# Kernel tuning notes

Measured on AMD Instinct MI355X. Metric: run time of the kernel, lower is better.

The kernel has to match this reference:

```python
import jax, jax.numpy as jnp
import numpy as np

BATCH = 4096
IN_CAPS = 64
OUT_CAPS = 16
IN_DIM = 64
OUT_DIM = 64
NUM_ITER = 3
LN_EPS = 1e-5


def setup_inputs() -> dict:
    key = jax.random.key(0)
    ks = jax.random.split(key, 13)
    n = lambda k, s: jax.random.normal(k, s, dtype=jnp.float32)
    return {
        "x_inp": n(ks[0], (BATCH, IN_CAPS, IN_DIM)),
        "W_A": n(ks[1], (IN_CAPS, IN_DIM)),
        "B_A": n(ks[2], (IN_CAPS,)),
        "W_F1": n(ks[3], (IN_CAPS, IN_DIM, IN_DIM)),
        "W_F2": n(ks[4], (OUT_CAPS, IN_DIM, OUT_DIM)),
        "B_F2": n(ks[5], (OUT_CAPS, OUT_DIM)),
        "W_G1": n(ks[6], (OUT_DIM, OUT_DIM)),
        "W_G2": n(ks[7], (OUT_CAPS, OUT_DIM, IN_DIM)),
        "B_G2": n(ks[8], (OUT_CAPS, IN_DIM)),
        "ln_gamma": jnp.ones((OUT_DIM,), jnp.float32),
        "ln_beta": jnp.zeros((OUT_DIM,), jnp.float32),
        "W_S": n(ks[9], (IN_CAPS, OUT_CAPS, IN_DIM)),
        "B_S": n(ks[10], (IN_CAPS, OUT_CAPS)),
        "beta_use": n(ks[11], (IN_CAPS, OUT_CAPS)),
        "beta_ign": n(ks[12], (IN_CAPS, OUT_CAPS)),
    }


def _layer_norm(x, gamma, beta):
    mu = jnp.mean(x, axis=-1, keepdims=True)
    var = jnp.var(x, axis=-1, keepdims=True)  # biased, matches torch LayerNorm
    return (x - mu) * jax.lax.rsqrt(var + LN_EPS) * gamma + beta


def reference(x_inp, W_A, B_A, W_F1, W_F2, B_F2, W_G1, W_G2, B_G2,
              ln_gamma, ln_beta, W_S, B_S, beta_use, beta_ign):
    B = x_inp.shape[0]
    inv_sqrt = np.float32(1.0 / np.sqrt(IN_DIM))
    # activation logits per input capsule: [B, in_caps]
    a_e = jnp.einsum('bif,if->bi', x_inp, W_A) * inv_sqrt + B_A
    f_a_e = jax.nn.sigmoid(a_e)  # loop-invariant
    # temp_F is loop-invariant: [B, in_caps, in_dim]
    temp_F = jnp.einsum('bif,ifh->bih', x_inp, W_F1) * inv_sqrt
    R_em = jnp.full((B, IN_CAPS, OUT_CAPS), 1.0 / OUT_CAPS, dtype=x_inp.dtype)
    x_out = None
    for _ in range(NUM_ITER):
        D_use = f_a_e[:, :, None] * R_em                      # [B,i,m]
        D_ign = f_a_e[:, :, None] - D_use                     # [B,i,m]
        phi_em = beta_use * D_use - beta_ign * D_ign          # [B,i,m]
        temp_F_routed = phi_em.sum(axis=-1)[:, :, None] * temp_F  # [B,i,h]
        x_out = jnp.einsum('bih,mhd->bmd', temp_F_routed, W_F2) + B_F2  # [B,m,d]
        x_out_norm = _layer_norm(x_out, ln_gamma, ln_beta)
        temp_G = jnp.einsum('bmd,dh->bmh', x_out_norm, W_G1)  # [B,m,d]
        x_inp_hat = jnp.einsum('bmh,mhi->bmi', temp_G, W_G2) + B_G2  # [B,m,f]
        consistency = jnp.einsum('bif,bmf,imf->bim', x_inp, x_inp_hat, W_S) + B_S
        R_em = jax.nn.softmax(consistency, axis=-1)  # exp(log_softmax)
    return x_out
```

## Files before the change

kernel.cpp:

```cpp
#include <hip/hip_runtime.h>
#include <math.h>

#define IC 64
#define OC 16
#define DIM 64

typedef __attribute__((ext_vector_type(8))) short bf16x8;
typedef __attribute__((ext_vector_type(4))) float f32x4;

__device__ __forceinline__ unsigned short f2bf(float f) {
    unsigned int b = __float_as_uint(f);
    b += 0x7fffu + ((b >> 16) & 1u);
    return (unsigned short)(b >> 16);
}
__device__ __forceinline__ float bf2f(unsigned short h) {
    return __uint_as_float(((unsigned int)h) << 16);
}

__global__ void kSetup(const float* __restrict__ W_F2, const float* __restrict__ W_S,
                       const float* __restrict__ B_S, const float* __restrict__ bu,
                       const float* __restrict__ bi_, const float* __restrict__ W_G1,
                       const float* __restrict__ W_G2,
                       float* __restrict__ WF2t, float* __restrict__ WSt2,
                       float* __restrict__ WG12,
                       float* __restrict__ BSt, float* __restrict__ cb,
                       float* __restrict__ db, float* __restrict__ eb)
{
    int e = blockIdx.x * 256 + threadIdx.x;
    {
        int h = e >> 10, m = (e >> 6) & 15, d = e & 63;
        WF2t[e] = W_F2[((size_t)m * 64 + h) * 64 + d];
    }
    {
        int m = e >> 12, fo = (e >> 8) & 15, i = (e >> 2) & 63, fi = e & 3;
        WSt2[e] = W_S[((size_t)i * 16 + m) * 64 + fo * 4 + fi];
    }
    {
        int m = e >> 12, d = (e >> 6) & 63, f = e & 63;
        const float* g1 = W_G1 + d * 64;
        const float* g2 = W_G2 + (size_t)m * 4096 + f;
        float a = 0.f;
#pragma unroll 8
        for (int h = 0; h < 64; h++) a += g1[h] * g2[h * 64];
        WG12[e] = a;
    }
    if (e < 1024) {
        int m = e >> 6, i = e & 63;
        BSt[e] = B_S[i * 16 + m];
        cb[e] = bu[e] + bi_[e];
    }
    if (e < 64) {
        float sc = 0.f, sd = 0.f;
        for (int m = 0; m < 16; m++) {
            sc += bu[e * 16 + m] + bi_[e * 16 + m];
            sd += bi_[e * 16 + m];
        }
        db[e] = sd;
        eb[e] = sc * (1.0f / 16.0f) - sd;
    }
}

__global__ __launch_bounds__(256, 4)
void kT(const float* __restrict__ x, const float* __restrict__ W_A,
        const float* __restrict__ B_A, const float* __restrict__ eb,
        float* __restrict__ xq, float* __restrict__ fa, float* __restrict__ phi)
{
    __shared__ float Xs[2 * 64 * 65];
    const int t = threadIdx.x;
    const int blk = blockIdx.x;

    const float4* x4 = (const float4*)x;
#pragma unroll
    for (int s = 0; s < 8; s++) {
        int p = s * 256 + t;
        float4 v = x4[(size_t)blk * 2048 + p];
        int b = p >> 10, i = (p >> 4) & 63, fo = p & 15;
        float* row = &Xs[(b * 64 + i) * 65 + fo * 4];
        row[0] = v.x; row[1] = v.y; row[2] = v.z; row[3] = v.w;
    }
    __syncthreads();

    const int lane = t & 63, w = t >> 6;
#pragma unroll
    for (int s = 0; s < 8; s++) {
        int idx = s * 4 + w;
        int b = idx >> 4, fo = idx & 15;
        const float* row = &Xs[(b * 64 + lane) * 65 + fo * 4];
        ((float4*)xq)[((size_t)(blk * 2 + b) * 16 + fo) * 64 + lane] =
            make_float4(row[0], row[1], row[2], row[3]);
    }

    {
        int p = t >> 1, h = t & 1;
        int b = p >> 6, i = p & 63;
        const float* row = &Xs[(b * 64 + i) * 65 + h * 32];
        const float* wa = W_A + i * 64 + h * 32;
        float v = 0.f;
#pragma unroll
        for (int j = 0; j < 32; j++) v += row[j] * wa[j];
        v += __shfl_xor(v, 1);
        if (h == 0) {
            float ae = v * 0.125f + B_A[i];
            float fv = 1.0f / (1.0f + expf(-ae));
            size_t o = (size_t)(blk * 2 + b) * 64 + i;
            fa[o] = fv;
            phi[o] = fv * eb[i];
        }
    }
}

__global__ __launch_bounds__(256, 4)
void kA(const float* __restrict__ x, const float* __restrict__ W_F1,
        float* __restrict__ tF)
{
    __shared__ unsigned short Ah[64][72], Al[64][72];
    __shared__ unsigned short Bh[64][72], Bl[64][72];
    const int i = blockIdx.y;
    const int b0 = blockIdx.x * 64;
    const int t = threadIdx.x;
    const int bl = t >> 2, q = t & 3;

    {
        const float* src = x + ((size_t)(b0 + bl) * IC + i) * DIM + q * 4;
#pragma unroll
        for (int j4 = 0; j4 < 4; j4++) {
            float4 v = *(const float4*)(src + j4 * 16);
            int f = q * 4 + j4 * 16;
            float vv[4] = {v.x, v.y, v.z, v.w};
            ushort4 h4, l4;
            unsigned short hh;
            hh = f2bf(vv[0]); h4.x = hh; l4.x = f2bf(vv[0] - bf2f(hh));
            hh = f2bf(vv[1]); h4.y = hh; l4.y = f2bf(vv[1] - bf2f(hh));
            hh = f2bf(vv[2]); h4.z = hh; l4.z = f2bf(vv[2] - bf2f(hh));
            hh = f2bf(vv[3]); h4.w = hh; l4.w = f2bf(vv[3] - bf2f(hh));
            *(ushort4*)&Ah[bl][f] = h4;
            *(ushort4*)&Al[bl][f] = l4;
        }
        const float* wsrc = W_F1 + ((size_t)i * DIM + bl) * DIM + q * 4;
#pragma unroll
        for (int j4 = 0; j4 < 4; j4++) {
            float4 v = *(const float4*)(wsrc + j4 * 16);
            int h0 = q * 4 + j4 * 16;
            float vv[4] = {v.x, v.y, v.z, v.w};
#pragma unroll
            for (int c = 0; c < 4; c++) {
                unsigned short hh = f2bf(vv[c]);
                Bh[h0 + c][bl] = hh;
                Bl[h0 + c][bl] = f2bf(vv[c] - bf2f(hh));
            }
        }
    }
    __syncthreads();

    const int w = t >> 6, lane = t & 63;
    const int fm = lane & 15, fq = lane >> 4;
    const int r0 = w * 16;
    f32x4 acc[4];
#pragma unroll
    for (int nt = 0; nt < 4; nt++) {
        acc[nt][0] = 0.f; acc[nt][1] = 0.f; acc[nt][2] = 0.f; acc[nt][3] = 0.f;
    }

#pragma unroll
    for (int ks = 0; ks < 2; ks++) {
        const int kk = ks * 32 + fq * 8;
        bf16x8 ah = *(const bf16x8*)&Ah[r0 + fm][kk];
        bf16x8 al = *(const bf16x8*)&Al[r0 + fm][kk];
#pragma unroll
        for (int nt = 0; nt < 4; nt++) {
            bf16x8 bh = *(const bf16x8*)&Bh[nt * 16 + fm][kk];
            bf16x8 bl2 = *(const bf16x8*)&Bl[nt * 16 + fm][kk];
            acc[nt] = __builtin_amdgcn_mfma_f32_16x16x32_bf16(ah, bh, acc[nt], 0, 0, 0);
            acc[nt] = __builtin_amdgcn_mfma_f32_16x16x32_bf16(ah, bl2, acc[nt], 0, 0, 0);
            acc[nt] = __builtin_amdgcn_mfma_f32_16x16x32_bf16(al, bh, acc[nt], 0, 0, 0);
        }
    }

#pragma unroll
    for (int nt = 0; nt < 4; nt++)
#pragma unroll
        for (int j = 0; j < 4; j++) {
            int row = r0 + fq * 4 + j;
            int col = nt * 16 + fm;
            tF[((size_t)(b0 + row) * IC + i) * DIM + col] = acc[nt][j] * 0.125f;
        }
}

__global__ __launch_bounds__(256, 4)
void kS(const float* __restrict__ phi, const float* __restrict__ tF,
        float* __restrict__ s)
{
    __shared__ float ph[4 * 64];
    const int t = threadIdx.x;
    const int b0 = blockIdx.x * 4;
    ph[t] = phi[(size_t)b0 * 64 + t];
    __syncthreads();

    const int w = t >> 6, lane = t & 63;
    const int ig = lane >> 4, hq = lane & 15;
    const int b = b0 + w;
    const float4* tf4 = (const float4*)(tF + ((size_t)b * 64 + ig * 16) * 64) + hq;
    float4 a = make_float4(0.f, 0.f, 0.f, 0.f);
#pragma unroll
    for (int k = 0; k < 16; k++) {
        float p = ph[w * 64 + ig * 16 + k];
        float4 v = tf4[k * 16];
        a.x += p * v.x; a.y += p * v.y; a.z += p * v.z; a.w += p * v.w;
    }
#pragma unroll
    for (int k = 16; k <= 32; k <<= 1) {
        a.x += __shfl_xor(a.x, k); a.y += __shfl_xor(a.y, k);
        a.z += __shfl_xor(a.z, k); a.w += __shfl_xor(a.w, k);
    }
    if (ig == 0)
        ((float4*)(s + (size_t)b * 64))[hq] = a;
}

__global__ __launch_bounds__(256, 4)
void kXG(const float* __restrict__ s, const float* __restrict__ WF2t,
         const float* __restrict__ B_F2, const float* __restrict__ WG12,
         const float* __restrict__ B_G2,
         const float* __restrict__ gam, const float* __restrict__ bet,
         float* __restrict__ xhat, float* __restrict__ out, const int last)
{
    __shared__ float A[64][68];
    __shared__ float Wb[64][68];
    const int b0 = blockIdx.x * 64;
    const int m = blockIdx.y;
    const int t = threadIdx.x;
    const int bl = t >> 2, q = t & 3;
    const int tr = t >> 4, tc = t & 15;

    {
        const float* src = s + (size_t)(b0 + bl) * DIM + q * 4;
#pragma unroll
        for (int j4 = 0; j4 < 4; j4++) {
            float4 v = *(const float4*)(src + j4 * 16);
            int f = q * 4 + j4 * 16;
            A[f + 0][bl] = v.x; A[f + 1][bl] = v.y;
            A[f + 2][bl] = v.z; A[f + 3][bl] = v.w;
        }
        const float* wsrc = WF2t + ((size_t)bl * OC + m) * DIM + q * 4;
#pragma unroll
        for (int j4 = 0; j4 < 4; j4++)
            *(float4*)&Wb[bl][q * 4 + j4 * 16] = *(const float4*)(wsrc + j4 * 16);
    }
    __syncthreads();

    float acc[4][4];
#pragma unroll
    for (int r = 0; r < 4; r++)
#pragma unroll
        for (int c = 0; c < 4; c++) acc[r][c] = 0.f;
#pragma unroll 8
    for (int k = 0; k < 64; k++) {
        float4 a = *(const float4*)&A[k][tr * 4];
        float4 w = *(const float4*)&Wb[k][tc * 4];
        float ar[4] = {a.x, a.y, a.z, a.w};
#pragma unroll
        for (int r = 0; r < 4; r++) {
            acc[r][0] += ar[r] * w.x; acc[r][1] += ar[r] * w.y;
            acc[r][2] += ar[r] * w.z; acc[r][3] += ar[r] * w.w;
        }
    }
    {
        float4 bf = *(const float4*)&B_F2[m * DIM + tc * 4];
#pragma unroll
        for (int r = 0; r < 4; r++) {
            acc[r][0] += bf.x; acc[r][1] += bf.y;
            acc[r][2] += bf.z; acc[r][3] += bf.w;
        }
    }
    if (last) {
#pragma unroll
        for (int r = 0; r < 4; r++)
            *(float4*)&out[((size_t)(b0 + tr * 4 + r) * OC + m) * DIM + tc * 4] =
                make_float4(acc[r][0], acc[r][1], acc[r][2], acc[r][3]);
        return;
    }
    {
        float4 gv = *(const float4*)&gam[tc * 4];
        float4 bv = *(const float4*)&bet[tc * 4];
#pragma unroll
        for (int r = 0; r < 4; r++) {
            float sum = acc[r][0] + acc[r][1] + acc[r][2] + acc[r][3];
            float sq = acc[r][0] * acc[r][0] + acc[r][1] * acc[r][1] +
                       acc[r][2] * acc[r][2] + acc[r][3] * acc[r][3];
#pragma unroll
            for (int k = 1; k <= 8; k <<= 1) {
                sum += __shfl_xor(sum, k);
                sq  += __shfl_xor(sq, k);
            }
            float mu = sum * (1.0f / 64.0f);
            float var = sq * (1.0f / 64.0f) - mu * mu;
            float rs = 1.0f / sqrtf(var + 1e-5f);
            acc[r][0] = (acc[r][0] - mu) * rs * gv.x + bv.x;
            acc[r][1] = (acc[r][1] - mu) * rs * gv.y + bv.y;
            acc[r][2] = (acc[r][2] - mu) * rs * gv.z + bv.z;
            acc[r][3] = (acc[r][3] - mu) * rs * gv.w + bv.w;
        }
    }
    __syncthreads();
    {
#pragma unroll
        for (int r = 0; r < 4; r++)
#pragma unroll
            for (int c = 0; c < 4; c++)
                A[tc * 4 + c][tr * 4 + r] = acc[r][c];
        const float* wsrc = WG12 + ((size_t)m * DIM + bl) * DIM + q * 4;
#pragma unroll
        for (int j4 = 0; j4 < 4; j4++)
            *(float4*)&Wb[bl][q * 4 + j4 * 16] = *(const float4*)(wsrc + j4 * 16);
    }
    __syncthreads();

    float xh[4][4];
    {
        float4 bg = *(const float4*)&B_G2[m * DIM + tc * 4];
#pragma unroll
        for (int r = 0; r < 4; r++) {
            xh[r][0] = bg.x; xh[r][1] = bg.y; xh[r][2] = bg.z; xh[r][3] = bg.w;
        }
    }
#pragma unroll 8
    for (int k = 0; k < 64; k++) {
        float4 a = *(const float4*)&A[k][tr * 4];
        float4 w = *(const float4*)&Wb[k][tc * 4];
        float ar[4] = {a.x, a.y, a.z, a.w};
#pragma unroll
        for (int r = 0; r < 4; r++) {
            xh[r][0] += ar[r] * w.x; xh[r][1] += ar[r] * w.y;
            xh[r][2] += ar[r] * w.z; xh[r][3] += ar[r] * w.w;
        }
    }
#pragma unroll
    for (int r = 0; r < 4; r++)
        *(float4*)&xhat[((size_t)(b0 + tr * 4 + r) * OC + m) * DIM + tc * 4] =
            make_float4(xh[r][0], xh[r][1], xh[r][2], xh[r][3]);
}

__global__ __launch_bounds__(256, 4)
void kC(const float* __restrict__ xq, const float* __restrict__ xhat,
        const float* __restrict__ WSt2, const float* __restrict__ BSt,
        const float* __restrict__ cb, const float* __restrict__ db,
        const float* __restrict__ fa, const float* __restrict__ tF,
        float* __restrict__ s)
{
    __shared__ float buf[4 * 64 * 17];
    __shared__ float phs[4][64];
    const int b0 = blockIdx.x * 4;
    const int t = threadIdx.x;
    const int w = t >> 6, lane = t & 63;

    {
        const float4* src = (const float4*)(xhat + (size_t)b0 * OC * DIM);
        float4* dst = (float4*)buf;
#pragma unroll
        for (int j = 0; j < 4; j++) dst[t + j * 256] = src[t + j * 256];
    }
    __syncthreads();

    float acc[4][4];
#pragma unroll
    for (int k = 0; k < 4; k++) {
        float bs = BSt[(w * 4 + k) * IC + lane];
#pragma unroll
        for (int g = 0; g < 4; g++) acc[g][k] = bs;
    }

    const float4* xq4 = (const float4*)xq;
    for (int fc = 0; fc < 64; fc += 8) {
        const int fo = fc >> 2;
        float wreg[4][8];
#pragma unroll
        for (int k = 0; k < 4; k++) {
            int m = w * 4 + k;
#pragma unroll
            for (int q2 = 0; q2 < 2; q2++) {
                float4 v = *(const float4*)&WSt2[(((size_t)m * 16 + fo + q2) * IC + lane) * 4];
                wreg[k][q2 * 4 + 0] = v.x; wreg[k][q2 * 4 + 1] = v.y;
                wreg[k][q2 * 4 + 2] = v.z; wreg[k][q2 * 4 + 3] = v.w;
            }
        }
#pragma unroll
        for (int g = 0; g < 4; g++) {
            float xr[8];
#pragma unroll
            for (int q2 = 0; q2 < 2; q2++) {
                float4 v = xq4[((size_t)(b0 + g) * 16 + fo + q2) * 64 + lane];
                xr[q2 * 4 + 0] = v.x; xr[q2 * 4 + 1] = v.y;
                xr[q2 * 4 + 2] = v.z; xr[q2 * 4 + 3] = v.w;
            }
#pragma unroll
            for (int k = 0; k < 4; k++) {
                int m = w * 4 + k;
                const float* hp = &buf[(g * OC + m) * DIM + fc];
                float hr[8];
#pragma unroll
                for (int q2 = 0; q2 < 2; q2++) {
                    float4 v = *(const float4*)(hp + q2 * 4);
                    hr[q2 * 4 + 0] = v.x; hr[q2 * 4 + 1] = v.y;
                    hr[q2 * 4 + 2] = v.z; hr[q2 * 4 + 3] = v.w;
                }
#pragma unroll
                for (int ff = 0; ff < 8; ff++)
                    acc[g][k] += xr[ff] * hr[ff] * wreg[k][ff];
            }
        }
    }
    __syncthreads();
#pragma unroll
    for (int g = 0; g < 4; g++)
#pragma unroll
        for (int k = 0; k < 4; k++)
            buf[(g * IC + lane) * 17 + w * 4 + k] = acc[g][k];
    __syncthreads();

    {
        int g = t >> 6, i = t & 63;
        const float* row = &buf[(g * IC + i) * 17];
        float v[16], mx = -1e30f;
#pragma unroll
        for (int m = 0; m < OC; m++) { v[m] = row[m]; mx = fmaxf(mx, v[m]); }
        float sum = 0.f;
#pragma unroll
        for (int m = 0; m < OC; m++) { v[m] = expf(v[m] - mx); sum += v[m]; }
        float inv = 1.0f / sum;
        float a2 = 0.f;
#pragma unroll
        for (int m = 0; m < OC; m++) a2 += v[m] * inv * cb[i * OC + m];
        phs[g][i] = fa[(size_t)(b0 + g) * IC + i] * (a2 - db[i]);
    }
    __syncthreads();

    {
        const int ig = lane >> 4, hq = lane & 15;
        const int b = b0 + w;
        const float4* tf4 = (const float4*)(tF + ((size_t)b * 64 + ig * 16) * 64) + hq;
        float4 a = make_float4(0.f, 0.f, 0.f, 0.f);
#pragma unroll
        for (int k = 0; k < 16; k++) {
            float p = phs[w][ig * 16 + k];
            float4 v = tf4[k * 16];
            a.x += p * v.x; a.y += p * v.y; a.z += p * v.z; a.w += p * v.w;
        }
#pragma unroll
        for (int k = 16; k <= 32; k <<= 1) {
            a.x += __shfl_xor(a.x, k); a.y += __shfl_xor(a.y, k);
            a.z += __shfl_xor(a.z, k); a.w += __shfl_xor(a.w, k);
        }
        if (ig == 0)
            ((float4*)(s + (size_t)b * 64))[hq] = a;
    }
}

extern "C" void kernel_launch(void* const* d_in, const int* in_sizes, int n_in,
                              void* d_out, int out_size, void* d_ws, size_t ws_size,
                              hipStream_t stream)
{
    const float* x    = (const float*)d_in[0];
    const float* W_A  = (const float*)d_in[1];
    const float* B_A  = (const float*)d_in[2];
    const float* W_F1 = (const float*)d_in[3];
    const float* W_F2 = (const float*)d_in[4];
    const float* B_F2 = (const float*)d_in[5];
    const float* W_G1 = (const float*)d_in[6];
    const float* W_G2 = (const float*)d_in[7];
    const float* B_G2 = (const float*)d_in[8];
    const float* gam  = (const float*)d_in[9];
    const float* bet  = (const float*)d_in[10];
    const float* W_S  = (const float*)d_in[11];
    const float* B_S  = (const float*)d_in[12];
    const float* bu   = (const float*)d_in[13];
    const float* bi_  = (const float*)d_in[14];

    float* ws   = (float*)d_ws;
    float* tF   = ws;
    float* xq   = tF + 16777216;
    float* fa   = xq + 16777216;
    float* phi  = fa + 262144;
    float* s    = phi + 262144;
    float* xhat = s + 262144;
    float* WF2t = xhat + 4194304;
    float* WSt2 = WF2t + 65536;
    float* WG12 = WSt2 + 65536;
    float* BSt  = WG12 + 65536;
    float* cb   = BSt + 1024;
    float* db   = cb + 1024;
    float* eb   = db + 64;
    float* out  = (float*)d_out;

    kSetup<<<256, 256, 0, stream>>>(W_F2, W_S, B_S, bu, bi_, W_G1, W_G2,
                                    WF2t, WSt2, WG12, BSt, cb, db, eb);
    kT<<<2048, 256, 0, stream>>>(x, W_A, B_A, eb, xq, fa, phi);
    kA<<<dim3(64, 64), 256, 0, stream>>>(x, W_F1, tF);
    kS<<<1024, 256, 0, stream>>>(phi, tF, s);
    for (int it = 0; it < 3; ++it) {
        kXG<<<dim3(64, 16), 256, 0, stream>>>(s, WF2t, B_F2, WG12, B_G2,
                                              gam, bet, xhat, out, it == 2 ? 1 : 0);
        if (it < 2)
            kC<<<1024, 256, 0, stream>>>(xq, xhat, WSt2, BSt, cb, db, fa, tF, s);
    }
}
```

Before: 307.7 us.

## Run kXG GEMMs on MFMA using split-bf16 (hi/lo) three-term emulation

Replaces the FP32 scalar FMA loops in kXG with bf16 MFMA 16x16x32 instructions. Each fp32 operand is split into high and low bf16 halves, and three products (hh, hl, lh) recover near-fp32 accuracy. The setup kernel now pre-splits and transposes W_F2 and the fused W_G1·W_G2 weights into bf16 hi/lo buffers. The aim is to cut ALU time in the per-iteration GEMMs, at the cost of extra conversion work and some loss of precision in the dropped lo·lo term.

```diff
diff --git a/kernel.cpp b/kernel.cpp
--- a/kernel.cpp
+++ b/kernel.cpp
@@ -21,15 +21,19 @@
                        const float* __restrict__ B_S, const float* __restrict__ bu,
                        const float* __restrict__ bi_, const float* __restrict__ W_G1,
                        const float* __restrict__ W_G2,
-                       float* __restrict__ WF2t, float* __restrict__ WSt2,
-                       float* __restrict__ WG12,
+                       float* __restrict__ WSt2,
+                       unsigned short* __restrict__ W1h, unsigned short* __restrict__ W1l,
+                       unsigned short* __restrict__ W2h, unsigned short* __restrict__ W2l,
                        float* __restrict__ BSt, float* __restrict__ cb,
                        float* __restrict__ db, float* __restrict__ eb)
 {
     int e = blockIdx.x * 256 + threadIdx.x;
     {
         int h = e >> 10, m = (e >> 6) & 15, d = e & 63;
-        WF2t[e] = W_F2[((size_t)m * 64 + h) * 64 + d];
+        float v = W_F2[((size_t)m * 64 + h) * 64 + d];
+        unsigned short hh = f2bf(v);
+        size_t o = ((size_t)m * 64 + d) * 64 + h;
+        W1h[o] = hh; W1l[o] = f2bf(v - bf2f(hh));
     }
     {
         int m = e >> 12, fo = (e >> 8) & 15, i = (e >> 2) & 63, fi = e & 3;
@@ -42,7 +46,9 @@
         float a = 0.f;
 #pragma unroll 8
         for (int h = 0; h < 64; h++) a += g1[h] * g2[h * 64];
-        WG12[e] = a;
+        unsigned short hh = f2bf(a);
+        size_t o = ((size_t)m * 64 + f) * 64 + d;
+        W2h[o] = hh; W2l[o] = f2bf(a - bf2f(hh));
     }
     if (e < 1024) {
         int m = e >> 6, i = e & 63;
@@ -217,75 +223,98 @@
 }
 
 __global__ __launch_bounds__(256, 4)
-void kXG(const float* __restrict__ s, const float* __restrict__ WF2t,
-         const float* __restrict__ B_F2, const float* __restrict__ WG12,
+void kXG(const float* __restrict__ s,
+         const unsigned short* __restrict__ W1h, const unsigned short* __restrict__ W1l,
+         const float* __restrict__ B_F2,
+         const unsigned short* __restrict__ W2h, const unsigned short* __restrict__ W2l,
          const float* __restrict__ B_G2,
          const float* __restrict__ gam, const float* __restrict__ bet,
          float* __restrict__ xhat, float* __restrict__ out, const int last)
 {
-    __shared__ float A[64][68];
-    __shared__ float Wb[64][68];
+    __shared__ unsigned short Ah[64][72], Al[64][72];
+    __shared__ unsigned short Bh[64][72], Bl[64][72];
     const int b0 = blockIdx.x * 64;
     const int m = blockIdx.y;
     const int t = threadIdx.x;
     const int bl = t >> 2, q = t & 3;
-    const int tr = t >> 4, tc = t & 15;
-
-    {
-        const float* src = s + (size_t)(b0 + bl) * DIM + q * 4;
+
+    {
+        const float* src = s + (size_t)(b0 + bl) * DIM + q * 16;
 #pragma unroll
         for (int j4 = 0; j4 < 4; j4++) {
-            float4 v = *(const float4*)(src + j4 * 16);
-            int f = q * 4 + j4 * 16;
-            A[f + 0][bl] = v.x; A[f + 1][bl] = v.y;
-            A[f + 2][bl] = v.z; A[f + 3][bl] = v.w;
-        }
-        const float* wsrc = WF2t + ((size_t)bl * OC + m) * DIM + q * 4;
-#pragma unroll
-        for (int j4 = 0; j4 < 4; j4++)
-            *(float4*)&Wb[bl][q * 4 + j4 * 16] = *(const float4*)(wsrc + j4 * 16);
-    }
-    __syncthreads();
-
-    float acc[4][4];
-#pragma unroll
-    for (int r = 0; r < 4; r++)
-#pragma unroll
-        for (int c = 0; c < 4; c++) acc[r][c] = 0.f;
-#pragma unroll 8
-    for (int k = 0; k < 64; k++) {
-        float4 a = *(const float4*)&A[k][tr * 4];
-        float4 w = *(const float4*)&Wb[k][tc * 4];
-        float ar[4] = {a.x, a.y, a.z, a.w};
-#pragma unroll
-        for (int r = 0; r < 4; r++) {
-            acc[r][0] += ar[r] * w.x; acc[r][1] += ar[r] * w.y;
-            acc[r][2] += ar[r] * w.z; acc[r][3] += ar[r] * w.w;
-        }
-    }
-    {
-        float4 bf = *(const float4*)&B_F2[m * DIM + tc * 4];
-#pragma unroll
-        for (int r = 0; r < 4; r++) {
-            acc[r][0] += bf.x; acc[r][1] += bf.y;
-            acc[r][2] += bf.z; acc[r][3] += bf.w;
-        }
-    }
+            float4 v = ((const float4*)src)[j4];
+            int f = q * 16 + j4 * 4;
+            float vv[4] = {v.x, v.y, v.z, v.w};
+            ushort4 h4, l4;
+            unsigned short hh;
+            hh = f2bf(vv[0]); h4.x = hh; l4.x = f2bf(vv[0] - bf2f(hh));
+            hh = f2bf(vv[1]); h4.y = hh; l4.y = f2bf(vv[1] - bf2f(hh));
+            hh = f2bf(vv[2]); h4.z = hh; l4.z = f2bf(vv[2] - bf2f(hh));
+            hh = f2bf(vv[3]); h4.w = hh; l4.w = f2bf(vv[3] - bf2f(hh));
+            *(ushort4*)&Ah[bl][f] = h4;
+            *(ushort4*)&Al[bl][f] = l4;
+        }
+        const size_t wo = ((size_t)m * 64 + bl) * 64 + q * 16;
+#pragma unroll
+        for (int part = 0; part < 2; part++) {
+            *(uint4*)&Bh[bl][q * 16 + part * 8] = *(const uint4*)(W1h + wo + part * 8);
+            *(uint4*)&Bl[bl][q * 16 + part * 8] = *(const uint4*)(W1l + wo + part * 8);
+        }
+    }
+    __syncthreads();
+
+    const int w = t >> 6, lane = t & 63;
+    const int fm = lane & 15, fq = lane >> 4;
+    const int r0 = w * 16;
+    f32x4 acc[4];
+#pragma unroll
+    for (int nt = 0; nt < 4; nt++) {
+        acc[nt][0] = 0.f; acc[nt][1] = 0.f; acc[nt][2] = 0.f; acc[nt][3] = 0.f;
+    }
+#pragma unroll
+    for (int ks = 0; ks < 2; ks++) {
+        const int kk = ks * 32 + fq * 8;
+        bf16x8 ah = *(const bf16x8*)&Ah[r0 + fm][kk];
+        bf16x8 al = *(const bf16x8*)&Al[r0 + fm][kk];
+#pragma unroll
+        for (int nt = 0; nt < 4; nt++) {
+            bf16x8 bh = *(const bf16x8*)&Bh[nt * 16 + fm][kk];
+            bf16x8 bl2 = *(const bf16x8*)&Bl[nt * 16 + fm][kk];
+            acc[nt] = __builtin_amdgcn_mfma_f32_16x16x32_bf16(ah, bh, acc[nt], 0, 0, 0);
+            acc[nt] = __builtin_amdgcn_mfma_f32_16x16x32_bf16(ah, bl2, acc[nt], 0, 0, 0);
+            acc[nt] = __builtin_amdgcn_mfma_f32_16x16x32_bf16(al, bh, acc[nt], 0, 0, 0);
+        }
+    }
+#pragma unroll
+    for (int nt = 0; nt < 4; nt++) {
+        float bf = B_F2[m * DIM + nt * 16 + fm];
+#pragma unroll
+        for (int j = 0; j < 4; j++) acc[nt][j] += bf;
+    }
+
     if (last) {
 #pragma unroll
-        for (int r = 0; r < 4; r++)
-            *(float4*)&out[((size_t)(b0 + tr * 4 + r) * OC + m) * DIM + tc * 4] =
-                make_float4(acc[r][0], acc[r][1], acc[r][2], acc[r][3]);
+        for (int nt = 0; nt < 4; nt++)
+#pragma unroll
+            for (int j = 0; j < 4; j++) {
+                int row = r0 + fq * 4 + j;
+                out[((size_t)(b0 + row) * OC + m) * DIM + nt * 16 + fm] = acc[nt][j];
+            }
         return;
     }
-    {
-        float4 gv = *(const float4*)&gam[tc * 4];
-        float4 bv = *(const float4*)&bet[tc * 4];
-#pragma unroll
-        for (int r = 0; r < 4; r++) {
-            float sum = acc[r][0] + acc[r][1] + acc[r][2] + acc[r][3];
-            float sq = acc[r][0] * acc[r][0] + acc[r][1] * acc[r][1] +
-                       acc[r][2] * acc[r][2] + acc[r][3] * acc[r][3];
+
+    {
+        float g4[4], b4[4];
+#pragma unroll
+        for (int nt = 0; nt < 4; nt++) {
+            g4[nt] = gam[nt * 16 + fm];
+            b4[nt] = bet[nt * 16 + fm];
+        }
+#pragma unroll
+        for (int j = 0; j < 4; j++) {
+            float sum = acc[0][j] + acc[1][j] + acc[2][j] + acc[3][j];
+            float sq = acc[0][j] * acc[0][j] + acc[1][j] * acc[1][j] +
+                       acc[2][j] * acc[2][j] + acc[3][j] * acc[3][j];
 #pragma unroll
             for (int k = 1; k <= 8; k <<= 1) {
                 sum += __shfl_xor(sum, k);
@@ -294,49 +323,60 @@
             float mu = sum * (1.0f / 64.0f);
             float var = sq * (1.0f / 64.0f) - mu * mu;
             float rs = 1.0f / sqrtf(var + 1e-5f);
-            acc[r][0] = (acc[r][0] - mu) * rs * gv.x + bv.x;
-            acc[r][1] = (acc[r][1] - mu) * rs * gv.y + bv.y;
-            acc[r][2] = (acc[r][2] - mu) * rs * gv.z + bv.z;
-            acc[r][3] = (acc[r][3] - mu) * rs * gv.w + bv.w;
-        }
-    }
-    __syncthreads();
-    {
-#pragma unroll
-        for (int r = 0; r < 4; r++)
-#pragma unroll
-            for (int c = 0; c < 4; c++)
-                A[tc * 4 + c][tr * 4 + r] = acc[r][c];
-        const float* wsrc = WG12 + ((size_t)m * DIM + bl) * DIM + q * 4;
-#pragma unroll
-        for (int j4 = 0; j4 < 4; j4++)
-            *(float4*)&Wb[bl][q * 4 + j4 * 16] = *(const float4*)(wsrc + j4 * 16);
-    }
-    __syncthreads();
-
-    float xh[4][4];
-    {
-        float4 bg = *(const float4*)&B_G2[m * DIM + tc * 4];
-#pragma unroll
-        for (int r = 0; r < 4; r++) {
-            xh[r][0] = bg.x; xh[r][1] = bg.y; xh[r][2] = bg.z; xh[r][3] = bg.w;
-        }
-    }
-#pragma unroll 8
-    for (int k = 0; k < 64; k++) {
-        float4 a = *(const float4*)&A[k][tr * 4];
-        float4 w = *(const float4*)&Wb[k][tc * 4];
-        float ar[4] = {a.x, a.y, a.z, a.w};
-#pragma unroll
-        for (int r = 0; r < 4; r++) {
-            xh[r][0] += ar[r] * w.x; xh[r][1] += ar[r] * w.y;
-            xh[r][2] += ar[r] * w.z; xh[r][3] += ar[r] * w.w;
-        }
-    }
-#pragma unroll
-    for (int r = 0; r < 4; r++)
-        *(float4*)&xhat[((size_t)(b0 + tr * 4 + r) * OC + m) * DIM + tc * 4] =
-            make_float4(xh[r][0], xh[r][1], xh[r][2], xh[r][3]);
+#pragma unroll
+            for (int nt = 0; nt < 4; nt++)
+                acc[nt][j] = (acc[nt][j] - mu) * rs * g4[nt] + b4[nt];
+        }
+    }
+    __syncthreads();
+
+    {
+#pragma unroll
+        for (int nt = 0; nt < 4; nt++)
+#pragma unroll
+            for (int j = 0; j < 4; j++) {
+                float v = acc[nt][j];
+                unsigned short hh = f2bf(v);
+                int row = r0 + fq * 4 + j, col = nt * 16 + fm;
+                Ah[row][col] = hh;
+                Al[row][col] = f2bf(v - bf2f(hh));
+            }
+        const size_t wo = ((size_t)m * 64 + bl) * 64 + q * 16;
+#pragma unroll
+        for (int part = 0; part < 2; part++) {
+            *(uint4*)&Bh[bl][q * 16 + part * 8] = *(const uint4*)(W2h + wo + part * 8);
+            *(uint4*)&Bl[bl][q * 16 + part * 8] = *(const uint4*)(W2l + wo + part * 8);
+        }
+    }
+    __syncthreads();
+
+    f32x4 xh[4];
+#pragma unroll
+    for (int nt = 0; nt < 4; nt++) {
+        float bg = B_G2[m * DIM + nt * 16 + fm];
+        xh[nt][0] = bg; xh[nt][1] = bg; xh[nt][2] = bg; xh[nt][3] = bg;
+    }
+#pragma unroll
+    for (int ks = 0; ks < 2; ks++) {
+        const int kk = ks * 32 + fq * 8;
+        bf16x8 ah = *(const bf16x8*)&Ah[r0 + fm][kk];
+        bf16x8 al = *(const bf16x8*)&Al[r0 + fm][kk];
+#pragma unroll
+        for (int nt = 0; nt < 4; nt++) {
+            bf16x8 bh = *(const bf16x8*)&Bh[nt * 16 + fm][kk];
+            bf16x8 bl2 = *(const bf16x8*)&Bl[nt * 16 + fm][kk];
+            xh[nt] = __builtin_amdgcn_mfma_f32_16x16x32_bf16(ah, bh, xh[nt], 0, 0, 0);
+            xh[nt] = __builtin_amdgcn_mfma_f32_16x16x32_bf16(ah, bl2, xh[nt], 0, 0, 0);
+            xh[nt] = __builtin_amdgcn_mfma_f32_16x16x32_bf16(al, bh, xh[nt], 0, 0, 0);
+        }
+    }
+#pragma unroll
+    for (int nt = 0; nt < 4; nt++)
+#pragma unroll
+        for (int j = 0; j < 4; j++) {
+            int row = r0 + fq * 4 + j;
+            xhat[((size_t)(b0 + row) * OC + m) * DIM + nt * 16 + fm] = xh[nt][j];
+        }
 }
 
 __global__ __launch_bounds__(256, 4)
@@ -481,22 +521,24 @@
     float* phi  = fa + 262144;
     float* s    = phi + 262144;
     float* xhat = s + 262144;
-    float* WF2t = xhat + 4194304;
-    float* WSt2 = WF2t + 65536;
-    float* WG12 = WSt2 + 65536;
-    float* BSt  = WG12 + 65536;
+    float* WSt2 = xhat + 4194304;
+    unsigned short* W1h = (unsigned short*)(WSt2 + 65536);
+    unsigned short* W1l = W1h + 65536;
+    unsigned short* W2h = W1l + 65536;
+    unsigned short* W2l = W2h + 65536;
+    float* BSt  = (float*)(W2l + 65536);
     float* cb   = BSt + 1024;
     float* db   = cb + 1024;
     float* eb   = db + 64;
     float* out  = (float*)d_out;
 
     kSetup<<<256, 256, 0, stream>>>(W_F2, W_S, B_S, bu, bi_, W_G1, W_G2,
-                                    WF2t, WSt2, WG12, BSt, cb, db, eb);
+                                    WSt2, W1h, W1l, W2h, W2l, BSt, cb, db, eb);
     kT<<<2048, 256, 0, stream>>>(x, W_A, B_A, eb, xq, fa, phi);
     kA<<<dim3(64, 64), 256, 0, stream>>>(x, W_F1, tF);
     kS<<<1024, 256, 0, stream>>>(phi, tF, s);
     for (int it = 0; it < 3; ++it) {
-        kXG<<<dim3(64, 16), 256, 0, stream>>>(s, WF2t, B_F2, WG12, B_G2,
+        kXG<<<dim3(64, 16), 256, 0, stream>>>(s, W1h, W1l, B_F2, W2h, W2l, B_G2,
                                               gam, bet, xhat, out, it == 2 ? 1 : 0);
         if (it < 2)
             kC<<<1024, 256, 0, stream>>>(xq, xhat, WSt2, BSt, cb, db, fa, tF, s);
```

Result: faster. 285.2 us (-7.3%).
